# Kernel tuning notes

Hardware: AMD Instinct MI355X
Metric: run time of the kernel (lower is better)

Reference implementation:

```python
import jax, jax.numpy as jnp
import numpy as np

N = 4096      # nodes (= attention seq_len)
D = 256       # dim_h
H = 4         # num_heads
HD = D // H   # head dim
E = 131072    # edges (avg degree 32)


def _ln(x, g, b, eps=1e-5):
    mu = jnp.mean(x, -1, keepdims=True)
    var = jnp.var(x, -1, keepdims=True)
    return (x - mu) * jax.lax.rsqrt(var + eps) * g + b


def setup_inputs() -> dict:
    key = jax.random.key(0)
    ks = jax.random.split(key, 10)
    s = 0.02
    nrm = lambda k, shape: jax.random.normal(k, shape, jnp.float32) * s
    return dict(
        x=jax.random.normal(ks[0], (N, D), jnp.float32),
        edge_index=jax.random.randint(ks[1], (2, E), 0, N, dtype=jnp.int32),
        W_gcn=nrm(ks[2], (D, D)), b_gcn=jnp.zeros((D,), jnp.float32),
        w_qkv=nrm(ks[3], (D, 3 * D)), b_qkv=jnp.zeros((3 * D,), jnp.float32),
        w_out=nrm(ks[4], (D, D)), b_out=jnp.zeros((D,), jnp.float32),
        g1l=jnp.ones((D,), jnp.float32), beta1l=jnp.zeros((D,), jnp.float32),
        g1a=jnp.ones((D,), jnp.float32), beta1a=jnp.zeros((D,), jnp.float32),
        W1=nrm(ks[5], (D, 2 * D)), bf1=jnp.zeros((2 * D,), jnp.float32),
        W2=nrm(ks[6], (2 * D, D)), bf2=jnp.zeros((D,), jnp.float32),
        g2=jnp.ones((D,), jnp.float32), beta2=jnp.zeros((D,), jnp.float32),
    )


def reference(x, edge_index, W_gcn, b_gcn, w_qkv, b_qkv, w_out, b_out,
              g1l, beta1l, g1a, beta1a, W1, bf1, W2, bf2, g2, beta2):
    n = x.shape[0]
    # --- GCNConv: sym-normalized aggregation with self loops ---
    loop = jnp.arange(n, dtype=edge_index.dtype)
    src = jnp.concatenate([edge_index[0], loop])
    dst = jnp.concatenate([edge_index[1], loop])
    deg = jax.ops.segment_sum(jnp.ones_like(src, x.dtype), dst, num_segments=n)
    dinv = jax.lax.rsqrt(deg)  # deg >= 1 thanks to self loops
    h = x @ W_gcn                                  # [N, D]
    msg = h[src] * (dinv[src] * dinv[dst])[:, None]  # gather + edge norm
    x_local = jax.ops.segment_sum(msg, dst, num_segments=n) + b_gcn
    x = _ln(x + x_local, g1l, beta1l)
    # --- Multi-head self-attention over all nodes (one sequence) ---
    qkv = x @ w_qkv + b_qkv
    q, k, v = jnp.split(qkv, 3, axis=-1)
    q = q.reshape(n, H, HD)
    k = k.reshape(n, H, HD)
    v = v.reshape(n, H, HD)
    scale = 1.0 / (HD ** 0.5)
    scores = jnp.einsum('nhd,mhd->hnm', q, k) * scale   # [H, N, N]
    attn = jax.nn.softmax(scores, axis=-1)
    x_attn = jnp.einsum('hnm,mhd->nhd', attn, v).reshape(n, D) @ w_out + b_out
    x = _ln(x + x_attn, g1a, beta1a)
    # --- FFN (D -> 2D -> D, ReLU) ---
    x_ffn = jax.nn.relu(x @ W1 + bf1) @ W2 + bf2
    return _ln(x + x_ffn, g2, beta2)
```

## Files before the change

kernel.cpp:

```cpp
#include <hip/hip_runtime.h>

typedef unsigned short u16;
typedef __bf16 bf16x8 __attribute__((ext_vector_type(8)));
typedef float f32x4 __attribute__((ext_vector_type(4)));
typedef float f32x16 __attribute__((ext_vector_type(16)));
typedef unsigned u32x4v __attribute__((ext_vector_type(4)));

__device__ __forceinline__ u16 f2u(float f) {
    unsigned u = __builtin_bit_cast(unsigned, f);
    return (u16)((u + 0x7FFFu + ((u >> 16) & 1u)) >> 16);
}

__device__ __forceinline__ float u2f(u16 h) {
    return __builtin_bit_cast(float, (unsigned)h << 16);
}

__device__ __forceinline__ void glds16(const u16* g, u16* l) {
    __builtin_amdgcn_global_load_lds((const __attribute__((address_space(1))) unsigned int*)g,
                                     (__attribute__((address_space(3))) unsigned int*)l, 16, 0, 0);
}


__global__ __launch_bounds__(256) void prep_k(
    const float* __restrict__ w0, const float* __restrict__ w1, const float* __restrict__ w2,
    const float* __restrict__ w3, const float* __restrict__ w4, const float* __restrict__ x,
    u16* __restrict__ o0, u16* __restrict__ o1, u16* __restrict__ o2,
    u16* __restrict__ o3, u16* __restrict__ o4, u16* __restrict__ xo,
    int* __restrict__ cnt, int xblocks, int nn) {
    int b = blockIdx.x, t = threadIdx.x;
    if (b < 144) {
        const float* in; u16* out; int R, C, tb;
        if (b < 16)       { in = w0; out = o0; R = 256; C = 256; tb = b; }
        else if (b < 64)  { in = w1; out = o1; R = 256; C = 768; tb = b - 16; }
        else if (b < 80)  { in = w2; out = o2; R = 256; C = 256; tb = b - 64; }
        else if (b < 112) { in = w3; out = o3; R = 256; C = 512; tb = b - 80; }
        else              { in = w4; out = o4; R = 512; C = 256; tb = b - 112; }
        int tcols = C >> 6;
        int tr = tb / tcols, tc = tb - tr * tcols;
        __shared__ float T[64][65];
        int i0 = t >> 6, j = t & 63;
#pragma unroll
        for (int p = 0; p < 16; p++) {
            int r = p * 4 + i0;
            T[r][j] = in[(long)(tr * 64 + r) * C + tc * 64 + j];
        }
        __syncthreads();
#pragma unroll
        for (int p = 0; p < 16; p++) {
            int c = p * 4 + i0;
            out[(long)(tc * 64 + c) * R + tr * 64 + j] = f2u(T[j][c]);
        }
    } else if (b < 144 + xblocks) {
        long base = (long)(b - 144) * 4096;
#pragma unroll
        for (int p = 0; p < 4; p++) {
            long idx = base + p * 1024 + t * 4;
            float4 v = *(const float4*)&x[idx];
            unsigned lo = (unsigned)f2u(v.x) | ((unsigned)f2u(v.y) << 16);
            unsigned hi = (unsigned)f2u(v.z) | ((unsigned)f2u(v.w) << 16);
            *(uint2*)&xo[idx] = uint2{lo, hi};
        }
    } else {
        int i = (b - 144 - xblocks) * 256 + t;
        if (i < nn) cnt[i] = 0;
    }
}


__device__ __forceinline__ void block_ln_stats(float v, float& mu, float& rstd) {
    float s1 = v, s2 = v * v;
#pragma unroll
    for (int m = 1; m < 64; m <<= 1) { s1 += __shfl_xor(s1, m, 64); s2 += __shfl_xor(s2, m, 64); }
    __shared__ float r1[4], r2[4];
    int lane = threadIdx.x & 63, w = threadIdx.x >> 6;
    if (lane == 0) { r1[w] = s1; r2[w] = s2; }
    __syncthreads();
    s1 = r1[0] + r1[1] + r1[2] + r1[3];
    s2 = r2[0] + r2[1] + r2[2] + r2[3];
    mu = s1 * (1.0f / 256.0f);
    float var = s2 * (1.0f / 256.0f) - mu * mu;
    rstd = rsqrtf(var + 1e-5f);
}


__global__ __launch_bounds__(256) void gcn_agg_ln_k(
    const u16* __restrict__ h, const float* __restrict__ x,
    const int* __restrict__ srcs, const int* __restrict__ cnt,
    const float* __restrict__ bg,
    const float* __restrict__ g, const float* __restrict__ be,
    float* __restrict__ x1, u16* __restrict__ x1bf) {
    int n = blockIdx.x, d = threadIdx.x;
    int c = cnt[n]; c = c < 128 ? c : 128;
    int st = n << 7;
    float dn = rsqrtf((float)(c + 1));
    float agg = u2f(h[(long)n * 256 + d]) * dn;
    int e = 0;
    for (; e + 4 <= c; e += 4) {
        int s0 = srcs[st + e], s1 = srcs[st + e + 1], s2 = srcs[st + e + 2], s3 = srcs[st + e + 3];
        float a0 = u2f(h[(long)s0 * 256 + d]) * rsqrtf((float)(cnt[s0] + 1));
        float a1 = u2f(h[(long)s1 * 256 + d]) * rsqrtf((float)(cnt[s1] + 1));
        float a2 = u2f(h[(long)s2 * 256 + d]) * rsqrtf((float)(cnt[s2] + 1));
        float a3 = u2f(h[(long)s3 * 256 + d]) * rsqrtf((float)(cnt[s3] + 1));
        agg += (a0 + a1) + (a2 + a3);
    }
    for (; e < c; e++) {
        int s = srcs[st + e];
        agg += u2f(h[(long)s * 256 + d]) * rsqrtf((float)(cnt[s] + 1));
    }
    float v = x[(long)n * 256 + d] + dn * agg + bg[d];
    float mu, rs;
    block_ln_stats(v, mu, rs);
    float y = (v - mu) * rs * g[d] + be[d];
    x1[(long)n * 256 + d] = y;
    x1bf[(long)n * 256 + d] = f2u(y);
}


template <int EPI>
__device__ __forceinline__ void gemm_body(
    int bx, int by,
    const u16* __restrict__ A, const u16* __restrict__ Bt,
    const float* __restrict__ bias, void* __restrict__ outp,
    int M, int N, int K) {
    __shared__ __align__(16) u16 As[64 * 256];
    __shared__ __align__(16) u16 Bs[64 * 256];
    int tid = threadIdx.x;
    int lane = tid & 63, w = tid >> 6;
    int l15 = lane & 15, quad = lane >> 4, l7 = l15 & 7;
    int m0 = bx * 64, n0 = by * 64;
    int wm = (w >> 1) * 32, wn = (w & 1) * 32;
    f32x4 acc[2][2];
#pragma unroll
    for (int i = 0; i < 2; i++)
#pragma unroll
        for (int j = 0; j < 2; j++) acc[i][j] = f32x4{0.f, 0.f, 0.f, 0.f};

    int rA0 = (wm + l15) * 256, rA1 = (wm + 16 + l15) * 256;
    int rB0 = (wn + l15) * 256, rB1 = (wn + 16 + l15) * 256;

    for (int kb = 0; kb < K; kb += 256) {
        if (kb) __syncthreads();
#pragma unroll
        for (int i = 0; i < 8; i++) {
            int s = i * 256 + tid;
            int j = s >> 5, dch = s & 31;
            int c = dch ^ (j & 7);
            glds16(A + (long)(m0 + j) * K + kb + c * 8, &As[s * 8]);
            glds16(Bt + (long)(n0 + j) * K + kb + c * 8, &Bs[s * 8]);
        }
        __syncthreads();
#pragma unroll
        for (int step = 0; step < 8; step++) {
            int d8 = (((step << 2) + quad) ^ l7) << 3;
            bf16x8 af0 = *(const bf16x8*)&As[rA0 + d8];
            bf16x8 af1 = *(const bf16x8*)&As[rA1 + d8];
            bf16x8 bf0 = *(const bf16x8*)&Bs[rB0 + d8];
            bf16x8 bf1 = *(const bf16x8*)&Bs[rB1 + d8];
            acc[0][0] = __builtin_amdgcn_mfma_f32_16x16x32_bf16(af0, bf0, acc[0][0], 0, 0, 0);
            acc[0][1] = __builtin_amdgcn_mfma_f32_16x16x32_bf16(af0, bf1, acc[0][1], 0, 0, 0);
            acc[1][0] = __builtin_amdgcn_mfma_f32_16x16x32_bf16(af1, bf0, acc[1][0], 0, 0, 0);
            acc[1][1] = __builtin_amdgcn_mfma_f32_16x16x32_bf16(af1, bf1, acc[1][1], 0, 0, 0);
        }
    }

#pragma unroll
    for (int nf = 0; nf < 2; nf++) {
        int col = n0 + wn + nf * 16 + l15;
        float bv = bias ? bias[col] : 0.0f;
#pragma unroll
        for (int mf = 0; mf < 2; mf++) {
#pragma unroll
            for (int r = 0; r < 4; r++) {
                int row = m0 + wm + mf * 16 + quad * 4 + r;
                float v = acc[mf][nf][r] + bv;
                if (EPI == 1) {
                    u16* q = (u16*)outp;
                    u16* kk = q + (long)M * 256;
                    u16* vt = kk + (long)M * 256;
                    if (col < 256) {
                        q[(((col >> 6) * (long)M) + row) * 64 + (col & 63)] = f2u(v * 0.180336884f);
                    } else if (col < 512) {
                        int c = col - 256;
                        kk[(((c >> 6) * (long)M) + row) * 64 + (c & 63)] = f2u(v);
                    } else {
                        int c = col - 512;
                        vt[((c >> 6) * 64 + (c & 63)) * (long)M + row] = f2u(v);
                    }
                } else if (EPI == 2) {
                    ((u16*)outp)[(long)row * N + col] = f2u(v > 0.f ? v : 0.f);
                } else {
                    ((u16*)outp)[(long)row * N + col] = f2u(v);
                }
            }
        }
    }
}

template <int EPI>
__global__ __launch_bounds__(256) void gemm_k(
    const u16* __restrict__ A, const u16* __restrict__ Bt,
    const float* __restrict__ bias, void* __restrict__ outp,
    int M, int N, int K) {
    gemm_body<EPI>(blockIdx.x, blockIdx.y, A, Bt, bias, outp, M, N, K);
}


template <int WRITE_BF>
__global__ __launch_bounds__(256) void gemm_ln_k(
    const u16* __restrict__ A, const u16* __restrict__ Bt, const float* __restrict__ bias,
    const float* __restrict__ res, const float* __restrict__ g, const float* __restrict__ be,
    float* __restrict__ outf, u16* __restrict__ outbf, int M, int K) {
    __shared__ __align__(16) u16 As[16 * 64];
    __shared__ __align__(16) u16 Bs[256 * 64];
    __shared__ float red[2][4][16];
    int tid = threadIdx.x;
    int lane = tid & 63, w = tid >> 6;
    int l15 = lane & 15, quad = lane >> 4, l7 = l15 & 7;
    int m0 = blockIdx.x * 16;
    f32x4 acc[4];
#pragma unroll
    for (int i = 0; i < 4; i++) acc[i] = f32x4{0.f, 0.f, 0.f, 0.f};

    int jA = tid >> 3, dA = tid & 7, cA = dA ^ (jA & 7);
    const u16* agp = A + (long)(m0 + jA) * K + cA * 8;

    for (int kb = 0; kb < K; kb += 64) {
        if (kb) __syncthreads();
        if (tid < 128) glds16(agp + kb, &As[tid * 8]);
#pragma unroll
        for (int i = 0; i < 8; i++) {
            int s = i * 256 + tid;
            int jb = s >> 3, db = s & 7, cb = db ^ (jb & 7);
            glds16(Bt + (long)jb * K + kb + cb * 8, &Bs[s * 8]);
        }
        __syncthreads();
#pragma unroll
        for (int step = 0; step < 2; step++) {
            int d8 = (((step << 2) + quad) ^ l7) << 3;
            bf16x8 af = *(const bf16x8*)&As[l15 * 64 + d8];
#pragma unroll
            for (int nf = 0; nf < 4; nf++) {
                int rb = w * 64 + nf * 16 + l15;
                bf16x8 bfr = *(const bf16x8*)&Bs[rb * 64 + d8];
                acc[nf] = __builtin_amdgcn_mfma_f32_16x16x32_bf16(af, bfr, acc[nf], 0, 0, 0);
            }
        }
    }

    float vv[4][4];
    float p1[4] = {0.f, 0.f, 0.f, 0.f}, p2[4] = {0.f, 0.f, 0.f, 0.f};
#pragma unroll
    for (int nf = 0; nf < 4; nf++) {
        int col = w * 64 + nf * 16 + l15;
        float bv = bias[col];
#pragma unroll
        for (int r = 0; r < 4; r++) {
            int row = m0 + quad * 4 + r;
            float v = acc[nf][r] + bv + res[(long)row * 256 + col];
            vv[nf][r] = v;
            p1[r] += v; p2[r] += v * v;
        }
    }
#pragma unroll
    for (int m = 1; m < 16; m <<= 1) {
#pragma unroll
        for (int r = 0; r < 4; r++) {
            p1[r] += __shfl_xor(p1[r], m, 64);
            p2[r] += __shfl_xor(p2[r], m, 64);
        }
    }
    if (l15 == 0) {
#pragma unroll
        for (int r = 0; r < 4; r++) { red[0][w][quad * 4 + r] = p1[r]; red[1][w][quad * 4 + r] = p2[r]; }
    }
    __syncthreads();
    float mu[4], rs[4];
#pragma unroll
    for (int r = 0; r < 4; r++) {
        int rr = quad * 4 + r;
        float s1 = red[0][0][rr] + red[0][1][rr] + red[0][2][rr] + red[0][3][rr];
        float s2 = red[1][0][rr] + red[1][1][rr] + red[1][2][rr] + red[1][3][rr];
        mu[r] = s1 * (1.0f / 256.0f);
        float var = s2 * (1.0f / 256.0f) - mu[r] * mu[r];
        rs[r] = rsqrtf(var + 1e-5f);
    }
#pragma unroll
    for (int nf = 0; nf < 4; nf++) {
        int col = w * 64 + nf * 16 + l15;
        float gg = g[col], bb = be[col];
#pragma unroll
        for (int r = 0; r < 4; r++) {
            int row = m0 + quad * 4 + r;
            float y = (vv[nf][r] - mu[r]) * rs[r] * gg + bb;
            outf[(long)row * 256 + col] = y;
            if (WRITE_BF) outbf[(long)row * 256 + col] = f2u(y);
        }
    }
}


__global__ __launch_bounds__(256) void comb_gemm_ln_k(
    const float* __restrict__ po, const float* __restrict__ pl,
    const u16* __restrict__ Bt, const float* __restrict__ bias,
    const float* __restrict__ res, const float* __restrict__ g, const float* __restrict__ be,
    float* __restrict__ outf, u16* __restrict__ outbf, int M, int S) {
    const int K = 256;
    __shared__ __align__(16) u16 As16[16 * 256];
    __shared__ __align__(16) u16 Bs[256 * 64];
    __shared__ float red[2][4][16];
    int tid = threadIdx.x;
    int lane = tid & 63, w = tid >> 6;
    int l15 = lane & 15, quad = lane >> 4, l7 = l15 & 7;
    int m0 = blockIdx.x * 16;

    {
        int d = lane;
        int g8 = w * 8 + (d >> 3), e = d & 7;
#pragma unroll
        for (int r = 0; r < 16; r++) {
            float osum = 0.f, lsum = 0.f;
            for (int s = 0; s < S; s++) {
                long pb = ((long)(s * 4 + w)) * M;
                osum += po[(pb + m0 + r) * 64 + d];
                lsum += pl[pb + m0 + r];
            }
            int slot = (g8 & ~7) | ((g8 & 7) ^ (r & 7));
            As16[r * 256 + slot * 8 + e] = f2u(osum / lsum);
        }
    }

    f32x4 acc[4];
#pragma unroll
    for (int i = 0; i < 4; i++) acc[i] = f32x4{0.f, 0.f, 0.f, 0.f};

    for (int kb = 0; kb < K; kb += 64) {
        if (kb) __syncthreads();
#pragma unroll
        for (int i = 0; i < 8; i++) {
            int s = i * 256 + tid;
            int jb = s >> 3, db = s & 7, cb = db ^ (jb & 7);
            glds16(Bt + (long)jb * K + kb + cb * 8, &Bs[s * 8]);
        }
        __syncthreads();
#pragma unroll
        for (int step = 0; step < 2; step++) {
            int d8 = (((step << 2) + quad) ^ l7) << 3;
            bf16x8 af = *(const bf16x8*)&As16[l15 * 256 + kb + d8];
#pragma unroll
            for (int nf = 0; nf < 4; nf++) {
                int rb = w * 64 + nf * 16 + l15;
                bf16x8 bfr = *(const bf16x8*)&Bs[rb * 64 + d8];
                acc[nf] = __builtin_amdgcn_mfma_f32_16x16x32_bf16(af, bfr, acc[nf], 0, 0, 0);
            }
        }
    }

    float vv[4][4];
    float p1[4] = {0.f, 0.f, 0.f, 0.f}, p2[4] = {0.f, 0.f, 0.f, 0.f};
#pragma unroll
    for (int nf = 0; nf < 4; nf++) {
        int col = w * 64 + nf * 16 + l15;
        float bv = bias[col];
#pragma unroll
        for (int r = 0; r < 4; r++) {
            int row = m0 + quad * 4 + r;
            float v = acc[nf][r] + bv + res[(long)row * 256 + col];
            vv[nf][r] = v;
            p1[r] += v; p2[r] += v * v;
        }
    }
#pragma unroll
    for (int m = 1; m < 16; m <<= 1) {
#pragma unroll
        for (int r = 0; r < 4; r++) {
            p1[r] += __shfl_xor(p1[r], m, 64);
            p2[r] += __shfl_xor(p2[r], m, 64);
        }
    }
    if (l15 == 0) {
#pragma unroll
        for (int r = 0; r < 4; r++) { red[0][w][quad * 4 + r] = p1[r]; red[1][w][quad * 4 + r] = p2[r]; }
    }
    __syncthreads();
    float mu[4], rs[4];
#pragma unroll
    for (int r = 0; r < 4; r++) {
        int rr = quad * 4 + r;
        float s1 = red[0][0][rr] + red[0][1][rr] + red[0][2][rr] + red[0][3][rr];
        float s2 = red[1][0][rr] + red[1][1][rr] + red[1][2][rr] + red[1][3][rr];
        mu[r] = s1 * (1.0f / 256.0f);
        float var = s2 * (1.0f / 256.0f) - mu[r] * mu[r];
        rs[r] = rsqrtf(var + 1e-5f);
    }
#pragma unroll
    for (int nf = 0; nf < 4; nf++) {
        int col = w * 64 + nf * 16 + l15;
        float gg = g[col], bb = be[col];
#pragma unroll
        for (int r = 0; r < 4; r++) {
            int row = m0 + quad * 4 + r;
            float y = (vv[nf][r] - mu[r]) * rs[r] * gg + bb;
            outf[(long)row * 256 + col] = y;
            outbf[(long)row * 256 + col] = f2u(y);
        }
    }
}


__global__ __launch_bounds__(256) void front_k(
    const int* __restrict__ ei, int E, int* __restrict__ cnt, int* __restrict__ srcs,
    const u16* __restrict__ A, const u16* __restrict__ Bt, void* __restrict__ outp,
    int M, int N, int K, int SB) {
    int b = blockIdx.x;
    if (b < SB) {
        int e = b * 256 + threadIdx.x;
        if (e < E) {
            int s = ei[e], d = ei[E + e];
            int p = atomicAdd(&cnt[d], 1);
            if (p < 128) srcs[(d << 7) + p] = s;
        }
    } else {
        int id = b - SB;
        gemm_body<3>(id & 63, id >> 6, A, Bt, nullptr, outp, M, N, K);
    }
}


__global__ __launch_bounds__(256) void attn_k(const u16* __restrict__ qg, const u16* __restrict__ kg,
                                              const u16* __restrict__ vtg, float* __restrict__ po,
                                              float* __restrict__ pl, int N, int S) {
    int tid = threadIdx.x;
    int w = tid >> 6, lane = tid & 63;
    int l31 = lane & 31, h = lane >> 5, xr = l31 & 7;
    int hh = blockIdx.y, sp = blockIdx.z;
    int q0w = blockIdx.x * 128 + w * 32;
    int kbeg = sp * (N / S);
    int nit = (N / S) / 64;
    const u16* qh = qg + (long)hh * N * 64;
    const u16* kh = kg + (long)hh * N * 64;
    const u16* vh = vtg + (long)hh * 64 * N;

    __shared__ __align__(16) u16 KV[2][2][4096];

    int s0 = tid, j0 = s0 >> 3, c0s = ((s0 & 7) ^ (j0 & 7)) * 8;
    int s1 = tid + 256, j1 = s1 >> 3, c1s = ((s1 & 7) ^ (j1 & 7)) * 8;
    const u16* kp0 = kh + (long)(kbeg + j0) * 64 + c0s;
    const u16* kp1 = kh + (long)(kbeg + j1) * 64 + c1s;
    const u16* vp0 = vh + (long)j0 * N + kbeg + c0s;
    const u16* vp1 = vh + (long)j1 * N + kbeg + c1s;
    u16* lk0[2] = {&KV[0][0][s0 * 8], &KV[1][0][s0 * 8]};
    u16* lk1[2] = {&KV[0][0][s1 * 8], &KV[1][0][s1 * 8]};
    u16* lv0[2] = {&KV[0][1][s0 * 8], &KV[1][1][s0 * 8]};
    u16* lv1[2] = {&KV[0][1][s1 * 8], &KV[1][1][s1 * 8]};

    bf16x8 qf[4];
#pragma unroll
    for (int stp = 0; stp < 4; stp++)
        qf[stp] = *(const bf16x8*)(qh + (long)(q0w + l31) * 64 + stp * 16 + h * 8);

    bf16x8 ones;
#pragma unroll
    for (int i = 0; i < 8; i++) ones[i] = (__bf16)1.0f;

    f32x16 o0{}, o1{}, accl{};

    glds16(kp0, lk0[0]); glds16(kp1, lk1[0]);
    glds16(vp0, lv0[0]); glds16(vp1, lv1[0]);
    kp0 += 4096; kp1 += 4096; vp0 += 64; vp1 += 64;

    for (int it = 0; it < nit; it++) {
        __syncthreads();
        if (it + 1 < nit) {
            int nb = (it + 1) & 1;
            glds16(kp0, lk0[nb]); glds16(kp1, lk1[nb]);
            glds16(vp0, lv0[nb]); glds16(vp1, lv1[nb]);
            kp0 += 4096; kp1 += 4096; vp0 += 64; vp1 += 64;
        }
        const u16* Kc = &KV[it & 1][0][0];
        const u16* Vc = &KV[it & 1][1][0];

        f32x16 sA{}, sB{};
#pragma unroll
        for (int stp = 0; stp < 4; stp++) {
            int cc = (((stp << 1) + h) ^ xr) * 8;
            bf16x8 kfa = *(const bf16x8*)&Kc[l31 * 64 + cc];
            bf16x8 kfb = *(const bf16x8*)&Kc[(32 + l31) * 64 + cc];
            sA = __builtin_amdgcn_mfma_f32_32x32x16_bf16(kfa, qf[stp], sA, 0, 0, 0);
            sB = __builtin_amdgcn_mfma_f32_32x32x16_bf16(kfb, qf[stp], sB, 0, 0, 0);
        }

#pragma unroll
        for (int kt = 0; kt < 2; kt++) {
            f32x16 s = kt ? sB : sA;
            unsigned wr[8];
#pragma unroll
            for (int i = 0; i < 8; i++) {
                unsigned ua = (unsigned)((int)(s[2 * i] * 8388608.0f) + 1064992209);
                unsigned ub = (unsigned)((int)(s[2 * i + 1] * 8388608.0f) + 1064992209);
                wr[i] = __builtin_amdgcn_perm(ub, ua, 0x07060302u);
            }
            asm("v_permlane32_swap_b32 %0, %1" : "+v"(wr[2]), "+v"(wr[0]));
            asm("v_permlane32_swap_b32 %0, %1" : "+v"(wr[3]), "+v"(wr[1]));
            asm("v_permlane32_swap_b32 %0, %1" : "+v"(wr[6]), "+v"(wr[4]));
            asm("v_permlane32_swap_b32 %0, %1" : "+v"(wr[7]), "+v"(wr[5]));
            u32x4v t0 = {wr[0], wr[1], wr[2], wr[3]};
            u32x4v t1 = {wr[4], wr[5], wr[6], wr[7]};
            bf16x8 f0 = __builtin_bit_cast(bf16x8, t0);
            bf16x8 f1 = __builtin_bit_cast(bf16x8, t1);

            accl = __builtin_amdgcn_mfma_f32_32x32x16_bf16(f0, ones, accl, 0, 0, 0);
            accl = __builtin_amdgcn_mfma_f32_32x32x16_bf16(f1, ones, accl, 0, 0, 0);

#pragma unroll
            for (int dt = 0; dt < 2; dt++) {
                int rowb = (dt * 32 + l31) * 64;
                bf16x8 v0 = *(const bf16x8*)&Vc[rowb + (((kt << 2) + h) ^ xr) * 8];
                bf16x8 v1 = *(const bf16x8*)&Vc[rowb + (((kt << 2) + 2 + h) ^ xr) * 8];
                if (dt == 0) {
                    o0 = __builtin_amdgcn_mfma_f32_32x32x16_bf16(f0, v0, o0, 0, 0, 0);
                    o0 = __builtin_amdgcn_mfma_f32_32x32x16_bf16(f1, v1, o0, 0, 0, 0);
                } else {
                    o1 = __builtin_amdgcn_mfma_f32_32x32x16_bf16(f0, v0, o1, 0, 0, 0);
                    o1 = __builtin_amdgcn_mfma_f32_32x32x16_bf16(f1, v1, o1, 0, 0, 0);
                }
            }
        }
    }

    long pbase = ((long)(sp * 4 + hh)) * N;
#pragma unroll
    for (int dt = 0; dt < 2; dt++)
#pragma unroll
        for (int r = 0; r < 16; r++) {
            int qrow = q0w + (r & 3) + ((r >> 2) << 3) + (h << 2);
            float val = dt ? o1[r] : o0[r];
            po[(pbase + qrow) * 64 + dt * 32 + l31] = val;
        }
    if (l31 == 0) {
#pragma unroll
        for (int r = 0; r < 16; r++) {
            int qrow = q0w + (r & 3) + ((r >> 2) << 3) + (h << 2);
            pl[pbase + qrow] = accl[r];
        }
    }
}


extern "C" void kernel_launch(void* const* d_in, const int* in_sizes, int n_in,
                              void* d_out, int out_size, void* d_ws, size_t ws_size,
                              hipStream_t stream) {
    const float* x    = (const float*)d_in[0];
    const int*   ei   = (const int*)d_in[1];
    const float* Wg   = (const float*)d_in[2];
    const float* bg   = (const float*)d_in[3];
    const float* Wqkv = (const float*)d_in[4];
    const float* bqkv = (const float*)d_in[5];
    const float* Wo   = (const float*)d_in[6];
    const float* bo   = (const float*)d_in[7];
    const float* g1l  = (const float*)d_in[8];
    const float* b1l  = (const float*)d_in[9];
    const float* g1a  = (const float*)d_in[10];
    const float* b1a  = (const float*)d_in[11];
    const float* W1   = (const float*)d_in[12];
    const float* bf1  = (const float*)d_in[13];
    const float* W2   = (const float*)d_in[14];
    const float* bf2  = (const float*)d_in[15];
    const float* g2   = (const float*)d_in[16];
    const float* b2   = (const float*)d_in[17];
    float* out = (float*)d_out;

    int N = in_sizes[0] / 256;
    int E = in_sizes[1] / 2;
    const int S = 4;

    char* p = (char*)d_ws;
    auto alloc = [&](size_t bytes) { void* r = (void*)p; p += (bytes + 255) & ~(size_t)255; return r; };
    u16*   wg_t   = (u16*)alloc((size_t)256 * 256 * 2);
    u16*   wqkv_t = (u16*)alloc((size_t)256 * 768 * 2);
    u16*   wo_t   = (u16*)alloc((size_t)256 * 256 * 2);
    u16*   w1_t   = (u16*)alloc((size_t)512 * 256 * 2);
    u16*   w2_t   = (u16*)alloc((size_t)256 * 512 * 2);
    u16*   xbf    = (u16*)alloc((size_t)N * 256 * 2);
    u16*   h      = (u16*)alloc((size_t)N * 256 * 2);
    int*   cnt    = (int*)alloc((size_t)N * 4);
    int*   srcs   = (int*)alloc((size_t)N * 128 * 4);
    float* x1     = (float*)alloc((size_t)N * 256 * 4);
    u16*   x1bf   = (u16*)alloc((size_t)N * 256 * 2);
    u16*   qkv    = (u16*)alloc((size_t)3 * N * 256 * 2);
    float* x2     = (float*)alloc((size_t)N * 256 * 4);
    u16*   x2bf   = (u16*)alloc((size_t)N * 256 * 2);
    u16*   ffn1   = (u16*)alloc((size_t)N * 512 * 2);
    float* po     = (float*)alloc((size_t)S * 4 * N * 64 * 4);
    float* pl     = (float*)alloc((size_t)S * 4 * N * 4);

    dim3 b256(256);

    int xblocks = (N * 256) / 4096;
    int cblocks = (N + 255) / 256;
    prep_k<<<144 + xblocks + cblocks, b256, 0, stream>>>(Wg, Wqkv, Wo, W1, W2, x,
                                                         wg_t, wqkv_t, wo_t, w1_t, w2_t, xbf,
                                                         cnt, xblocks, N);

    int SB = (E + 255) / 256;
    front_k<<<SB + (N / 64) * 4, b256, 0, stream>>>(ei, E, cnt, srcs, xbf, wg_t, h, N, 256, 256, SB);

    gcn_agg_ln_k<<<N, b256, 0, stream>>>(h, x, srcs, cnt, bg, g1l, b1l, x1, x1bf);

    gemm_k<1><<<dim3(N / 64, 12), b256, 0, stream>>>(x1bf, wqkv_t, bqkv, qkv, N, 768, 256);
    attn_k<<<dim3(N / 128, 4, S), b256, 0, stream>>>(qkv, qkv + (size_t)N * 256, qkv + (size_t)2 * N * 256,
                                                     po, pl, N, S);

    comb_gemm_ln_k<<<N / 16, b256, 0, stream>>>(po, pl, wo_t, bo, x1, g1a, b1a, x2, x2bf, N, S);

    gemm_k<2><<<dim3(N / 64, 8), b256, 0, stream>>>(x2bf, w1_t, bf1, ffn1, N, 512, 256);

    gemm_ln_k<0><<<N / 16, b256, 0, stream>>>(ffn1, w2_t, bf2, x2, g2, b2, out, nullptr, N, 512);
}
```

Measured before the change: 202.0 us.

## Fuse FFN into one kernel, split attention wider, use bf16 partials and scalar row sums

The two FFN GEMMs are fused into one kernel that keeps the ReLU hidden tile in LDS, so the N×512 intermediate no longer goes through global memory. Attention now uses 8 key splits instead of 4 and stores partial outputs in bf16. Softmax row sums are accumulated as scalars plus a cross-lane shuffle, replacing the MFMA-with-ones. The split-combine moves into a separate small kernel feeding the existing gemm_ln_k for the output projection. The generic GEMM's K tile is halved to 128 to cut LDS use per block, and the extra kernel and partial-buffer traffic are the added costs.

Measured after the change: 190.4 us. 1.06x faster.

```diff
diff --git a/kernel.cpp b/kernel.cpp
--- a/kernel.cpp
+++ b/kernel.cpp
@@ -122,8 +122,8 @@
     const u16* __restrict__ A, const u16* __restrict__ Bt,
     const float* __restrict__ bias, void* __restrict__ outp,
     int M, int N, int K) {
-    __shared__ __align__(16) u16 As[64 * 256];
-    __shared__ __align__(16) u16 Bs[64 * 256];
+    __shared__ __align__(16) u16 As[64 * 128];
+    __shared__ __align__(16) u16 Bs[64 * 128];
     int tid = threadIdx.x;
     int lane = tid & 63, w = tid >> 6;
     int l15 = lane & 15, quad = lane >> 4, l7 = l15 & 7;
@@ -135,22 +135,22 @@
 #pragma unroll
         for (int j = 0; j < 2; j++) acc[i][j] = f32x4{0.f, 0.f, 0.f, 0.f};
 
-    int rA0 = (wm + l15) * 256, rA1 = (wm + 16 + l15) * 256;
-    int rB0 = (wn + l15) * 256, rB1 = (wn + 16 + l15) * 256;
-
-    for (int kb = 0; kb < K; kb += 256) {
+    int rA0 = (wm + l15) * 128, rA1 = (wm + 16 + l15) * 128;
+    int rB0 = (wn + l15) * 128, rB1 = (wn + 16 + l15) * 128;
+
+    for (int kb = 0; kb < K; kb += 128) {
         if (kb) __syncthreads();
 #pragma unroll
-        for (int i = 0; i < 8; i++) {
+        for (int i = 0; i < 4; i++) {
             int s = i * 256 + tid;
-            int j = s >> 5, dch = s & 31;
+            int j = s >> 4, dch = s & 15;
             int c = dch ^ (j & 7);
             glds16(A + (long)(m0 + j) * K + kb + c * 8, &As[s * 8]);
             glds16(Bt + (long)(n0 + j) * K + kb + c * 8, &Bs[s * 8]);
         }
         __syncthreads();
 #pragma unroll
-        for (int step = 0; step < 8; step++) {
+        for (int step = 0; step < 4; step++) {
             int d8 = (((step << 2) + quad) ^ l7) << 3;
             bf16x8 af0 = *(const bf16x8*)&As[rA0 + d8];
             bf16x8 af1 = *(const bf16x8*)&As[rA1 + d8];
@@ -186,8 +186,6 @@
                         int c = col - 512;
                         vt[((c >> 6) * 64 + (c & 63)) * (long)M + row] = f2u(v);
                     }
-                } else if (EPI == 2) {
-                    ((u16*)outp)[(long)row * N + col] = f2u(v > 0.f ? v : 0.f);
                 } else {
                     ((u16*)outp)[(long)row * N + col] = f2u(v);
                 }
@@ -299,53 +297,81 @@
 }
 
 
-__global__ __launch_bounds__(256) void comb_gemm_ln_k(
-    const float* __restrict__ po, const float* __restrict__ pl,
-    const u16* __restrict__ Bt, const float* __restrict__ bias,
+__global__ __launch_bounds__(256) void ffn_fused_k(
+    const u16* __restrict__ A, const u16* __restrict__ W1t, const float* __restrict__ b1,
+    const u16* __restrict__ W2t, const float* __restrict__ b2v,
     const float* __restrict__ res, const float* __restrict__ g, const float* __restrict__ be,
-    float* __restrict__ outf, u16* __restrict__ outbf, int M, int S) {
-    const int K = 256;
-    __shared__ __align__(16) u16 As16[16 * 256];
+    float* __restrict__ outf, int M) {
+    __shared__ __align__(16) u16 As[16 * 64];
     __shared__ __align__(16) u16 Bs[256 * 64];
+    __shared__ __align__(16) u16 Hs[16 * 512];
     __shared__ float red[2][4][16];
     int tid = threadIdx.x;
     int lane = tid & 63, w = tid >> 6;
     int l15 = lane & 15, quad = lane >> 4, l7 = l15 & 7;
     int m0 = blockIdx.x * 16;
 
-    {
-        int d = lane;
-        int g8 = w * 8 + (d >> 3), e = d & 7;
-#pragma unroll
-        for (int r = 0; r < 16; r++) {
-            float osum = 0.f, lsum = 0.f;
-            for (int s = 0; s < S; s++) {
-                long pb = ((long)(s * 4 + w)) * M;
-                osum += po[(pb + m0 + r) * 64 + d];
-                lsum += pl[pb + m0 + r];
-            }
-            int slot = (g8 & ~7) | ((g8 & 7) ^ (r & 7));
-            As16[r * 256 + slot * 8 + e] = f2u(osum / lsum);
+    int jA = tid >> 3, dA = tid & 7, cA = dA ^ (jA & 7);
+    const u16* agp = A + (long)(m0 + jA) * 256 + cA * 8;
+
+#pragma unroll
+    for (int hf = 0; hf < 2; hf++) {
+        f32x4 acc[4];
+#pragma unroll
+        for (int i = 0; i < 4; i++) acc[i] = f32x4{0.f, 0.f, 0.f, 0.f};
+        for (int kb = 0; kb < 256; kb += 64) {
+            if (hf | kb) __syncthreads();
+            if (tid < 128) glds16(agp + kb, &As[tid * 8]);
+#pragma unroll
+            for (int i = 0; i < 8; i++) {
+                int s = i * 256 + tid;
+                int jb = s >> 3, db = s & 7, cb = db ^ (jb & 7);
+                glds16(W1t + (long)(hf * 256 + jb) * 256 + kb + cb * 8, &Bs[s * 8]);
+            }
+            __syncthreads();
+#pragma unroll
+            for (int step = 0; step < 2; step++) {
+                int d8 = (((step << 2) + quad) ^ l7) << 3;
+                bf16x8 af = *(const bf16x8*)&As[l15 * 64 + d8];
+#pragma unroll
+                for (int nf = 0; nf < 4; nf++) {
+                    int rb = w * 64 + nf * 16 + l15;
+                    bf16x8 bfr = *(const bf16x8*)&Bs[rb * 64 + d8];
+                    acc[nf] = __builtin_amdgcn_mfma_f32_16x16x32_bf16(af, bfr, acc[nf], 0, 0, 0);
+                }
+            }
+        }
+#pragma unroll
+        for (int nf = 0; nf < 4; nf++) {
+            int col = hf * 256 + w * 64 + nf * 16 + l15;
+            float bv = b1[col];
+            int g8 = col >> 3, e = col & 7;
+#pragma unroll
+            for (int r = 0; r < 4; r++) {
+                int row = quad * 4 + r;
+                float v = acc[nf][r] + bv;
+                int slot = (g8 & ~7) | ((g8 & 7) ^ (row & 7));
+                Hs[row * 512 + slot * 8 + e] = f2u(v > 0.f ? v : 0.f);
+            }
         }
     }
 
     f32x4 acc[4];
 #pragma unroll
     for (int i = 0; i < 4; i++) acc[i] = f32x4{0.f, 0.f, 0.f, 0.f};
-
-    for (int kb = 0; kb < K; kb += 64) {
-        if (kb) __syncthreads();
+    for (int kb = 0; kb < 512; kb += 64) {
+        __syncthreads();
 #pragma unroll
         for (int i = 0; i < 8; i++) {
             int s = i * 256 + tid;
             int jb = s >> 3, db = s & 7, cb = db ^ (jb & 7);
-            glds16(Bt + (long)jb * K + kb + cb * 8, &Bs[s * 8]);
+            glds16(W2t + (long)jb * 512 + kb + cb * 8, &Bs[s * 8]);
         }
         __syncthreads();
 #pragma unroll
         for (int step = 0; step < 2; step++) {
             int d8 = (((step << 2) + quad) ^ l7) << 3;
-            bf16x8 af = *(const bf16x8*)&As16[l15 * 256 + kb + d8];
+            bf16x8 af = *(const bf16x8*)&Hs[l15 * 512 + kb + d8];
 #pragma unroll
             for (int nf = 0; nf < 4; nf++) {
                 int rb = w * 64 + nf * 16 + l15;
@@ -360,7 +386,7 @@
 #pragma unroll
     for (int nf = 0; nf < 4; nf++) {
         int col = w * 64 + nf * 16 + l15;
-        float bv = bias[col];
+        float bv = b2v[col];
 #pragma unroll
         for (int r = 0; r < 4; r++) {
             int row = m0 + quad * 4 + r;
@@ -399,9 +425,7 @@
 #pragma unroll
         for (int r = 0; r < 4; r++) {
             int row = m0 + quad * 4 + r;
-            float y = (vv[nf][r] - mu[r]) * rs[r] * gg + bb;
-            outf[(long)row * 256 + col] = y;
-            outbf[(long)row * 256 + col] = f2u(y);
+            outf[(long)row * 256 + col] = (vv[nf][r] - mu[r]) * rs[r] * gg + bb;
         }
     }
 }
@@ -427,13 +451,13 @@
 
 
 __global__ __launch_bounds__(256) void attn_k(const u16* __restrict__ qg, const u16* __restrict__ kg,
-                                              const u16* __restrict__ vtg, float* __restrict__ po,
+                                              const u16* __restrict__ vtg, u16* __restrict__ po,
                                               float* __restrict__ pl, int N, int S) {
     int tid = threadIdx.x;
     int w = tid >> 6, lane = tid & 63;
     int l31 = lane & 31, h = lane >> 5, xr = l31 & 7;
-    int hh = blockIdx.y, sp = blockIdx.z;
-    int q0w = blockIdx.x * 128 + w * 32;
+    int qb = blockIdx.x, hh = blockIdx.y, sp = blockIdx.z;
+    int q0w = qb * 128 + w * 32;
     int kbeg = sp * (N / S);
     int nit = (N / S) / 64;
     const u16* qh = qg + (long)hh * N * 64;
@@ -458,11 +482,8 @@
     for (int stp = 0; stp < 4; stp++)
         qf[stp] = *(const bf16x8*)(qh + (long)(q0w + l31) * 64 + stp * 16 + h * 8);
 
-    bf16x8 ones;
-#pragma unroll
-    for (int i = 0; i < 8; i++) ones[i] = (__bf16)1.0f;
-
-    f32x16 o0{}, o1{}, accl{};
+    f32x16 o0{}, o1{};
+    float ll = 0.f;
 
     glds16(kp0, lk0[0]); glds16(kp1, lk1[0]);
     glds16(vp0, lv0[0]); glds16(vp1, lv1[0]);
@@ -497,6 +518,8 @@
             for (int i = 0; i < 8; i++) {
                 unsigned ua = (unsigned)((int)(s[2 * i] * 8388608.0f) + 1064992209);
                 unsigned ub = (unsigned)((int)(s[2 * i + 1] * 8388608.0f) + 1064992209);
+                ll += __builtin_bit_cast(float, ua & 0xffff0000u);
+                ll += __builtin_bit_cast(float, ub & 0xffff0000u);
                 wr[i] = __builtin_amdgcn_perm(ub, ua, 0x07060302u);
             }
             asm("v_permlane32_swap_b32 %0, %1" : "+v"(wr[2]), "+v"(wr[0]));
@@ -507,9 +530,6 @@
             u32x4v t1 = {wr[4], wr[5], wr[6], wr[7]};
             bf16x8 f0 = __builtin_bit_cast(bf16x8, t0);
             bf16x8 f1 = __builtin_bit_cast(bf16x8, t1);
-
-            accl = __builtin_amdgcn_mfma_f32_32x32x16_bf16(f0, ones, accl, 0, 0, 0);
-            accl = __builtin_amdgcn_mfma_f32_32x32x16_bf16(f1, ones, accl, 0, 0, 0);
 
 #pragma unroll
             for (int dt = 0; dt < 2; dt++) {
@@ -527,6 +547,7 @@
         }
     }
 
+    ll += __shfl_xor(ll, 32, 64);
     long pbase = ((long)(sp * 4 + hh)) * N;
 #pragma unroll
     for (int dt = 0; dt < 2; dt++)
@@ -534,15 +555,21 @@
         for (int r = 0; r < 16; r++) {
             int qrow = q0w + (r & 3) + ((r >> 2) << 3) + (h << 2);
             float val = dt ? o1[r] : o0[r];
-            po[(pbase + qrow) * 64 + dt * 32 + l31] = val;
-        }
-    if (l31 == 0) {
-#pragma unroll
-        for (int r = 0; r < 16; r++) {
-            int qrow = q0w + (r & 3) + ((r >> 2) << 3) + (h << 2);
-            pl[pbase + qrow] = accl[r];
-        }
-    }
+            po[(pbase + qrow) * 64 + dt * 32 + l31] = f2u(val);
+        }
+    if (lane < 32) pl[pbase + q0w + lane] = ll;
+}
+
+__global__ __launch_bounds__(256) void attn_comb_k(const u16* __restrict__ po, const float* __restrict__ pl,
+                                                   u16* __restrict__ xo, int N, int S) {
+    int n = blockIdx.x, c = threadIdx.x;
+    int hh = c >> 6, d = c & 63;
+    float osum = 0.f, lsum = 0.f;
+    for (int s = 0; s < S; s++) {
+        osum += u2f(po[(((long)(s * 4 + hh)) * N + n) * 64 + d]);
+        lsum += pl[((long)(s * 4 + hh)) * N + n];
+    }
+    xo[(long)n * 256 + c] = f2u(osum / lsum);
 }
 
 
@@ -571,7 +598,7 @@
 
     int N = in_sizes[0] / 256;
     int E = in_sizes[1] / 2;
-    const int S = 4;
+    const int S = 8;
 
     char* p = (char*)d_ws;
     auto alloc = [&](size_t bytes) { void* r = (void*)p; p += (bytes + 255) & ~(size_t)255; return r; };
@@ -587,10 +614,10 @@
     float* x1     = (float*)alloc((size_t)N * 256 * 4);
     u16*   x1bf   = (u16*)alloc((size_t)N * 256 * 2);
     u16*   qkv    = (u16*)alloc((size_t)3 * N * 256 * 2);
+    u16*   xattn  = (u16*)alloc((size_t)N * 256 * 2);
     float* x2     = (float*)alloc((size_t)N * 256 * 4);
     u16*   x2bf   = (u16*)alloc((size_t)N * 256 * 2);
-    u16*   ffn1   = (u16*)alloc((size_t)N * 512 * 2);
-    float* po     = (float*)alloc((size_t)S * 4 * N * 64 * 4);
+    u16*   po     = (u16*)alloc((size_t)S * 4 * N * 64 * 2);
     float* pl     = (float*)alloc((size_t)S * 4 * N * 4);
 
     dim3 b256(256);
@@ -607,12 +634,12 @@
     gcn_agg_ln_k<<<N, b256, 0, stream>>>(h, x, srcs, cnt, bg, g1l, b1l, x1, x1bf);
 
     gemm_k<1><<<dim3(N / 64, 12), b256, 0, stream>>>(x1bf, wqkv_t, bqkv, qkv, N, 768, 256);
+
     attn_k<<<dim3(N / 128, 4, S), b256, 0, stream>>>(qkv, qkv + (size_t)N * 256, qkv + (size_t)2 * N * 256,
                                                      po, pl, N, S);
-
-    comb_gemm_ln_k<<<N / 16, b256, 0, stream>>>(po, pl, wo_t, bo, x1, g1a, b1a, x2, x2bf, N, S);
-
-    gemm_k<2><<<dim3(N / 64, 8), b256, 0, stream>>>(x2bf, w1_t, bf1, ffn1, N, 512, 256);
-
-    gemm_ln_k<0><<<N / 16, b256, 0, stream>>>(ffn1, w2_t, bf2, x2, g2, b2, out, nullptr, N, 512);
-}
+    attn_comb_k<<<N, b256, 0, stream>>>(po, pl, xattn, N, S);
+
+    gemm_ln_k<1><<<N / 16, b256, 0, stream>>>(xattn, wo_t, bo, x1, g1a, b1a, x2, x2bf, N, 256);
+
+    ffn_fused_k<<<N / 16, b256, 0, stream>>>(x2bf, w1_t, bf1, w2_t, bf2, x2, g2, b2, out, N);
+}
```
